# Performance work log

Measured on AMD Instinct MI355X. Metric: run time of the kernel, lower is better.

The kernel has to match this reference:

```python
import jax, jax.numpy as jnp
import numpy as np
import math

EMBED_DIM = 1024
NUM_HEADS = 16
D_K = EMBED_DIM // NUM_HEADS  # 64 qubits per head
BATCH, SEQ = 4, 2048


def setup_inputs() -> dict:
    key = jax.random.key(0)
    k_x, k_th, k_w, k_b = jax.random.split(key, 4)
    x = jax.random.normal(k_x, (BATCH, SEQ, EMBED_DIM), dtype=jnp.float32)
    # trainable RX angle per head per qubit (tq.RX has one param each)
    theta = jax.random.normal(k_th, (NUM_HEADS, D_K), dtype=jnp.float32)
    # out_linear
    lim = 1.0 / math.sqrt(EMBED_DIM)
    w_out = jax.random.uniform(k_w, (EMBED_DIM, EMBED_DIM), jnp.float32, -lim, lim)
    b_out = jax.random.uniform(k_b, (EMBED_DIM,), jnp.float32, -lim, lim)
    return {"x": x, "theta": theta, "w_out": w_out, "b_out": b_out}


def reference(x, theta, w_out, b_out):
    B, S, E = x.shape
    H, d_k = theta.shape
    # Quantum head: RX(x_i) then RX(theta_i) on |0>, measure PauliZ ->
    # <Z_i> = cos(x_i + theta_i). No entangling gates in the code path.
    ang = x.reshape(B, S, H, d_k) + theta  # broadcast [H,d_k]
    qkv = jnp.cos(ang).transpose(0, 2, 1, 3)  # [B,H,S,d_k]; Q == K == V
    scale = 1.0 / math.sqrt(d_k)
    scores = jnp.einsum('bhqd,bhkd->bhqk', qkv, qkv) * scale
    attn = jax.nn.softmax(scores, axis=-1)  # dropout is identity in eval
    out = jnp.einsum('bhqk,bhkd->bhqd', attn, qkv)
    out = out.transpose(0, 2, 1, 3).reshape(B, S, E)
    return out @ w_out.T + b_out
```

## Files before the change

### kernel.cpp

```cpp
#include <hip/hip_runtime.h>


#define B_  4
#define S_  2048
#define H_  16
#define D_  64
#define E_  1024
#define EXP2_SCALE 0.18033688011112043f

typedef unsigned short u16;
typedef unsigned int u32;
typedef __attribute__((ext_vector_type(8))) short short8;
typedef __attribute__((ext_vector_type(4))) float floatx4;

static __device__ __forceinline__ float bf2f(u16 v) {
    return __uint_as_float(((unsigned)v) << 16);
}
static __device__ __forceinline__ u16 f2bf(float f) {
    unsigned u = __float_as_uint(f);
    return (u16)((u + 0x7FFFu + ((u >> 16) & 1u)) >> 16);
}
static __device__ __forceinline__ u32 pack_bf16_trunc(float lo, float hi) {
    return __builtin_amdgcn_perm(__float_as_uint(hi), __float_as_uint(lo), 0x07060302u);
}
static __device__ __forceinline__ short8 scale8(short8 v) {
    short8 o;
#pragma unroll
    for (int i = 0; i < 8; i++)
        o[i] = (short)f2bf(bf2f((u16)v[i]) * EXP2_SCALE);
    return o;
}

#define KSWZ(r, c) ((((r)) << 6) + (((c) ^ ((((r)) & 7) << 3))))

__global__ __launch_bounds__(256) void prep_kernel(const float* __restrict__ x,
                                                   const float* __restrict__ theta,
                                                   const float* __restrict__ W,
                                                   u16* __restrict__ qkv,
                                                   u16* __restrict__ qkvT,
                                                   u16* __restrict__ Wb) {
    __shared__ __align__(16) u16 TQ[64][72];
    int blk = blockIdx.x;
    int tid = threadIdx.x;
    if (blk >= 2048) {
        int i = ((blk - 2048) * 256 + tid) * 4;
        float4 w = *(const float4*)(W + i);
        ushort4 o;
        o.x = f2bf(w.x); o.y = f2bf(w.y); o.z = f2bf(w.z); o.w = f2bf(w.w);
        *(ushort4*)(Wb + i) = o;
        return;
    }
    int stile = blk & 31;
    int bh    = blk >> 5;
    int b     = bh >> 4;
    int h     = bh & 15;
    int i     = tid >> 2;
    int d0    = (tid & 3) << 4;
    int s0    = stile << 6;
    int s     = s0 + i;

    const float* xp = x + ((size_t)(b * S_ + s)) * E_ + h * D_ + d0;
    const float* tp = theta + h * D_ + d0;

    u16 ov[16];
#pragma unroll
    for (int j = 0; j < 16; j += 4) {
        float4 xv = *(const float4*)(xp + j);
        float4 tv = *(const float4*)(tp + j);
        ov[j]     = f2bf(__cosf(xv.x + tv.x));
        ov[j + 1] = f2bf(__cosf(xv.y + tv.y));
        ov[j + 2] = f2bf(__cosf(xv.z + tv.z));
        ov[j + 3] = f2bf(__cosf(xv.w + tv.w));
    }

    u16* qp = qkv + ((size_t)bh * S_ + s) * D_ + d0;
    *(uint4*)qp       = *(uint4*)&ov[0];
    *(uint4*)(qp + 8) = *(uint4*)&ov[8];

#pragma unroll
    for (int j = 0; j < 16; j++) TQ[d0 + j][i] = ov[j];
    __syncthreads();

    int d  = tid >> 2;
    int j0 = (tid & 3) << 4;
    u16 tmp[16];
#pragma unroll
    for (int j = 0; j < 16; j++) tmp[j] = TQ[d][j0 + j];
    u16* qtp = qkvT + ((size_t)bh * D_ + d) * S_ + s0 + j0;
    *(uint4*)qtp       = *(uint4*)&tmp[0];
    *(uint4*)(qtp + 8) = *(uint4*)&tmp[8];
}

__global__ __launch_bounds__(256, 4) void attn_kernel(const u16* __restrict__ qkv,
                                                      const u16* __restrict__ qkvT,
                                                      u16* __restrict__ aout) {
    int blk0 = blockIdx.x;
    int blk  = (blk0 & 7) * 128 + (blk0 >> 3);
    int qt   = blk & 15;
    int bh   = blk >> 4;
    int b    = bh >> 4;
    int h    = bh & 15;
    int tid  = threadIdx.x;
    int wave = tid >> 6;
    int lane = tid & 63;
    int lq   = lane & 15;
    int lg   = lane >> 4;
    int r    = tid >> 2;
    int c0   = (tid & 3) << 4;

    __shared__ __align__(16) u16 Kt[64 * 64];
    __shared__ __align__(16) u16 Vt[64 * 64];
    __shared__ __align__(16) u16 Pb[4][32 * 64];

    const u16* base  = qkv  + (size_t)bh * S_ * D_;
    const u16* baseT = qkvT + (size_t)bh * D_ * S_;
    int s0 = qt * 128;

    short8 bq[2][2];
#pragma unroll
    for (int rf = 0; rf < 2; rf++) {
        const u16* qrow = base + (size_t)(s0 + wave * 32 + rf * 16 + lq) * D_ + lg * 8;
        bq[rf][0] = scale8(*(const short8*)qrow);
        bq[rf][1] = scale8(*(const short8*)(qrow + 32));
    }

    floatx4 oacc[2][4] = {{{0,0,0,0},{0,0,0,0},{0,0,0,0},{0,0,0,0}},
                          {{0,0,0,0},{0,0,0,0},{0,0,0,0},{0,0,0,0}}};
    float lsum[2] = {0.f, 0.f};

    {
        const u16* p = base + (size_t)r * D_ + c0;
        *(uint4*)&Kt[KSWZ(r, c0)]     = *(const uint4*)p;
        *(uint4*)&Kt[KSWZ(r, c0 + 8)] = *(const uint4*)(p + 8);
        const u16* p2 = baseT + (size_t)r * S_ + c0;
        *(uint4*)&Vt[KSWZ(r, c0)]     = *(const uint4*)p2;
        *(uint4*)&Vt[KSWZ(r, c0 + 8)] = *(const uint4*)(p2 + 8);
    }
    __syncthreads();

    for (int kt = 0; kt < S_ / 64; kt++) {
        uint4 nk0, nk1, nv0, nv1;
        if (kt < S_ / 64 - 1) {
            const u16* p = base + (size_t)((kt + 1) * 64 + r) * D_ + c0;
            nk0 = *(const uint4*)p;
            nk1 = *(const uint4*)(p + 8);
            const u16* p2 = baseT + (size_t)r * S_ + (kt + 1) * 64 + c0;
            nv0 = *(const uint4*)p2;
            nv1 = *(const uint4*)(p2 + 8);
        }

        floatx4 sc[2][4];
        __builtin_amdgcn_s_setprio(1);
#pragma unroll
        for (int t = 0; t < 4; t++) {
            short8 a0 = *(short8*)&Kt[KSWZ(t * 16 + lq, lg * 8)];
            short8 a1 = *(short8*)&Kt[KSWZ(t * 16 + lq, 32 + lg * 8)];
#pragma unroll
            for (int rf = 0; rf < 2; rf++) {
                floatx4 acc = {0, 0, 0, 0};
                acc = __builtin_amdgcn_mfma_f32_16x16x32_bf16(a0, bq[rf][0], acc, 0, 0, 0);
                sc[rf][t] = __builtin_amdgcn_mfma_f32_16x16x32_bf16(a1, bq[rf][1], acc, 0, 0, 0);
            }
        }
        __builtin_amdgcn_s_setprio(0);

#pragma unroll
        for (int rf = 0; rf < 2; rf++) {
#pragma unroll
            for (int t = 0; t < 4; t++) {
                float p0 = __builtin_amdgcn_exp2f(sc[rf][t][0]);
                float p1 = __builtin_amdgcn_exp2f(sc[rf][t][1]);
                float p2 = __builtin_amdgcn_exp2f(sc[rf][t][2]);
                float p3 = __builtin_amdgcn_exp2f(sc[rf][t][3]);
                lsum[rf] += (p0 + p1) + (p2 + p3);
                uint2 w;
                w.x = pack_bf16_trunc(p0, p1);
                w.y = pack_bf16_trunc(p2, p3);
                *(uint2*)&Pb[wave][KSWZ(rf * 16 + lq, t * 16 + lg * 4)] = w;
            }
        }

        asm volatile("s_waitcnt lgkmcnt(0)" ::: "memory");

        short8 bp[2][2];
#pragma unroll
        for (int rf = 0; rf < 2; rf++) {
            bp[rf][0] = *(short8*)&Pb[wave][KSWZ(rf * 16 + lq, lg * 8)];
            bp[rf][1] = *(short8*)&Pb[wave][KSWZ(rf * 16 + lq, 32 + lg * 8)];
        }
        __builtin_amdgcn_s_setprio(1);
#pragma unroll
        for (int t = 0; t < 4; t++) {
            short8 av0 = *(short8*)&Vt[KSWZ(t * 16 + lq, lg * 8)];
            short8 av1 = *(short8*)&Vt[KSWZ(t * 16 + lq, 32 + lg * 8)];
#pragma unroll
            for (int rf = 0; rf < 2; rf++) {
                oacc[rf][t] = __builtin_amdgcn_mfma_f32_16x16x32_bf16(av0, bp[rf][0], oacc[rf][t], 0, 0, 0);
                oacc[rf][t] = __builtin_amdgcn_mfma_f32_16x16x32_bf16(av1, bp[rf][1], oacc[rf][t], 0, 0, 0);
            }
        }
        __builtin_amdgcn_s_setprio(0);

        __syncthreads();
        if (kt < S_ / 64 - 1) {
            *(uint4*)&Kt[KSWZ(r, c0)]     = nk0;
            *(uint4*)&Kt[KSWZ(r, c0 + 8)] = nk1;
            *(uint4*)&Vt[KSWZ(r, c0)]     = nv0;
            *(uint4*)&Vt[KSWZ(r, c0 + 8)] = nv1;
            __syncthreads();
        }
    }

#pragma unroll
    for (int rf = 0; rf < 2; rf++) {
        lsum[rf] += __shfl_xor(lsum[rf], 16);
        lsum[rf] += __shfl_xor(lsum[rf], 32);
    }
#pragma unroll
    for (int rf = 0; rf < 2; rf++) {
        float inv = 1.0f / fmaxf(lsum[rf], 1e-20f);
        int srow = s0 + wave * 32 + rf * 16 + lq;
        u16* arow = aout + ((size_t)(b * S_ + srow)) * E_ + h * D_;
#pragma unroll
        for (int t = 0; t < 4; t++)
#pragma unroll
            for (int rr = 0; rr < 4; rr++)
                arow[t * 16 + lg * 4 + rr] = f2bf(oacc[rf][t][rr] * inv);
    }
}

__global__ __launch_bounds__(256) void proj_kernel(const u16* __restrict__ A,
                                                   const u16* __restrict__ Wb,
                                                   const float* __restrict__ bias,
                                                   float* __restrict__ out) {
    int m0   = blockIdx.x * 128;
    int n0   = blockIdx.y * 128;
    int tid  = threadIdx.x;
    int wave = tid >> 6;
    int wm   = wave >> 1;
    int wn   = wave & 1;
    int lane = tid & 63;
    int lq   = lane & 15;
    int lg   = lane >> 4;
    int r    = tid >> 1;
    int c0   = (tid & 1) * 32;

    __shared__ __align__(16) u16 As[128][72];
    __shared__ __align__(16) u16 Bs[128][72];

    floatx4 acc[4][4];
#pragma unroll
    for (int i = 0; i < 4; i++)
#pragma unroll
        for (int j = 0; j < 4; j++) acc[i][j] = (floatx4){0, 0, 0, 0};

    for (int kc = 0; kc < E_; kc += 64) {
        __syncthreads();
        const u16* pa = A + (size_t)(m0 + r) * E_ + kc + c0;
        const u16* pw = Wb + (size_t)(n0 + r) * E_ + kc + c0;
#pragma unroll
        for (int j = 0; j < 4; j++) {
            *(uint4*)&As[r][c0 + j * 8] = *(const uint4*)(pa + j * 8);
            *(uint4*)&Bs[r][c0 + j * 8] = *(const uint4*)(pw + j * 8);
        }
        __syncthreads();

#pragma unroll
        for (int c = 0; c < 2; c++) {
            short8 af[4], bf[4];
#pragma unroll
            for (int i = 0; i < 4; i++)
                af[i] = *(short8*)&As[wm * 64 + i * 16 + lq][c * 32 + lg * 8];
#pragma unroll
            for (int j = 0; j < 4; j++)
                bf[j] = *(short8*)&Bs[wn * 64 + j * 16 + lq][c * 32 + lg * 8];
#pragma unroll
            for (int i = 0; i < 4; i++)
#pragma unroll
                for (int j = 0; j < 4; j++)
                    acc[i][j] = __builtin_amdgcn_mfma_f32_16x16x32_bf16(af[i], bf[j], acc[i][j], 0, 0, 0);
        }
    }

#pragma unroll
    for (int j = 0; j < 4; j++) {
        int nidx = n0 + wn * 64 + j * 16 + lq;
        float bv = bias[nidx];
#pragma unroll
        for (int i = 0; i < 4; i++) {
#pragma unroll
            for (int rr = 0; rr < 4; rr++) {
                int row = m0 + wm * 64 + i * 16 + lg * 4 + rr;
                out[(size_t)row * E_ + nidx] = acc[i][j][rr] + bv;
            }
        }
    }
}

extern "C" void kernel_launch(void* const* d_in, const int* in_sizes, int n_in,
                              void* d_out, int out_size, void* d_ws, size_t ws_size,
                              hipStream_t stream) {
    const float* x     = (const float*)d_in[0];
    const float* theta = (const float*)d_in[1];
    const float* w_out = (const float*)d_in[2];
    const float* b_out = (const float*)d_in[3];
    float* out = (float*)d_out;

    char* ws = (char*)d_ws;
    const size_t QKV_BYTES = (size_t)B_ * H_ * S_ * D_ * sizeof(u16);
    u16* qkv  = (u16*)ws;
    u16* qkvT = (u16*)(ws + QKV_BYTES);
    u16* aout = (u16*)(ws + 2 * QKV_BYTES);
    u16* wbf_safe = (u16*)(ws + 3 * QKV_BYTES);

    prep_kernel<<<3072, 256, 0, stream>>>(x, theta, w_out, qkv, qkvT, wbf_safe);
    attn_kernel<<<(B_ * H_) * (S_ / 128), 256, 0, stream>>>(qkv, qkvT, aout);
    dim3 pg(B_ * S_ / 128, E_ / 128);
    proj_kernel<<<pg, 256, 0, stream>>>(aout, wbf_safe, b_out, out);
}
```

Baseline: 198.4 us.

## Drop register prefetch of next K/V tile and interleave exp with QK MFMAs

Removes the register-staged prefetch of the next K and V tiles, loading them from global memory right after the barrier and storing them straight into LDS. The score computation now applies exp2 and packs P for each key sub-tile immediately, instead of holding all eight score accumulators, and the setprio hints around the QK MFMAs are dropped. This lowers register pressure, which may help occupancy, but global-load latency is no longer hidden behind compute and sits on the critical path each iteration.

```diff
diff --git a/kernel.cpp b/kernel.cpp
--- a/kernel.cpp
+++ b/kernel.cpp
@@ -139,39 +139,23 @@
     __syncthreads();
 
     for (int kt = 0; kt < S_ / 64; kt++) {
-        uint4 nk0, nk1, nv0, nv1;
-        if (kt < S_ / 64 - 1) {
-            const u16* p = base + (size_t)((kt + 1) * 64 + r) * D_ + c0;
-            nk0 = *(const uint4*)p;
-            nk1 = *(const uint4*)(p + 8);
-            const u16* p2 = baseT + (size_t)r * S_ + (kt + 1) * 64 + c0;
-            nv0 = *(const uint4*)p2;
-            nv1 = *(const uint4*)(p2 + 8);
-        }
-
-        floatx4 sc[2][4];
-        __builtin_amdgcn_s_setprio(1);
 #pragma unroll
         for (int t = 0; t < 4; t++) {
             short8 a0 = *(short8*)&Kt[KSWZ(t * 16 + lq, lg * 8)];
             short8 a1 = *(short8*)&Kt[KSWZ(t * 16 + lq, 32 + lg * 8)];
+            floatx4 sct[2];
 #pragma unroll
             for (int rf = 0; rf < 2; rf++) {
                 floatx4 acc = {0, 0, 0, 0};
                 acc = __builtin_amdgcn_mfma_f32_16x16x32_bf16(a0, bq[rf][0], acc, 0, 0, 0);
-                sc[rf][t] = __builtin_amdgcn_mfma_f32_16x16x32_bf16(a1, bq[rf][1], acc, 0, 0, 0);
+                sct[rf] = __builtin_amdgcn_mfma_f32_16x16x32_bf16(a1, bq[rf][1], acc, 0, 0, 0);
             }
-        }
-        __builtin_amdgcn_s_setprio(0);
-
-#pragma unroll
-        for (int rf = 0; rf < 2; rf++) {
-#pragma unroll
-            for (int t = 0; t < 4; t++) {
-                float p0 = __builtin_amdgcn_exp2f(sc[rf][t][0]);
-                float p1 = __builtin_amdgcn_exp2f(sc[rf][t][1]);
-                float p2 = __builtin_amdgcn_exp2f(sc[rf][t][2]);
-                float p3 = __builtin_amdgcn_exp2f(sc[rf][t][3]);
+#pragma unroll
+            for (int rf = 0; rf < 2; rf++) {
+                float p0 = __builtin_amdgcn_exp2f(sct[rf][0]);
+                float p1 = __builtin_amdgcn_exp2f(sct[rf][1]);
+                float p2 = __builtin_amdgcn_exp2f(sct[rf][2]);
+                float p3 = __builtin_amdgcn_exp2f(sct[rf][3]);
                 lsum[rf] += (p0 + p1) + (p2 + p3);
                 uint2 w;
                 w.x = pack_bf16_trunc(p0, p1);
@@ -203,12 +187,18 @@
 
         __syncthreads();
         if (kt < S_ / 64 - 1) {
-            *(uint4*)&Kt[KSWZ(r, c0)]     = nk0;
-            *(uint4*)&Kt[KSWZ(r, c0 + 8)] = nk1;
-            *(uint4*)&Vt[KSWZ(r, c0)]     = nv0;
-            *(uint4*)&Vt[KSWZ(r, c0 + 8)] = nv1;
-            __syncthreads();
-        }
+            const u16* p = base + (size_t)((kt + 1) * 64 + r) * D_ + c0;
+            uint4 k0 = *(const uint4*)p;
+            uint4 k1 = *(const uint4*)(p + 8);
+            const u16* p2 = baseT + (size_t)r * S_ + (kt + 1) * 64 + c0;
+            uint4 v0 = *(const uint4*)p2;
+            uint4 v1 = *(const uint4*)(p2 + 8);
+            *(uint4*)&Kt[KSWZ(r, c0)]     = k0;
+            *(uint4*)&Kt[KSWZ(r, c0 + 8)] = k1;
+            *(uint4*)&Vt[KSWZ(r, c0)]     = v0;
+            *(uint4*)&Vt[KSWZ(r, c0 + 8)] = v1;
+        }
+        __syncthreads();
     }
 
 #pragma unroll
```

Measured after the change: 196.2 us. Within noise of the previous version (-1.1%).
